# Performance work log

Measured on AMD Instinct MI355X. Metric: run time of the kernel, lower is better.

The kernel has to match this reference:

```python
import jax, jax.numpy as jnp
import numpy as np

NUM_USERS = 200000
NUM_ITEMS = 100000
EMBED_DIM = 64
N_LAYERS = 3
NNZ = 6000000
BATCH = 16384
N_NODES = NUM_USERS + NUM_ITEMS


def setup_inputs() -> dict:
    key = jax.random.key(0)
    k1, k2, k3, k4, k5, k6, k7 = jax.random.split(key, 7)
    user_emb = 0.01 * jax.random.normal(k1, (NUM_USERS, EMBED_DIM), dtype=jnp.float32)
    item_emb = 0.01 * jax.random.normal(k2, (NUM_ITEMS, EMBED_DIM), dtype=jnp.float32)
    adj_rows = jax.random.randint(k3, (NNZ,), 0, N_NODES, dtype=jnp.int32)
    adj_cols = jax.random.randint(k4, (NNZ,), 0, N_NODES, dtype=jnp.int32)
    # positive normalized-adjacency-like values (roughly 1/deg scale)
    adj_vals = jax.random.uniform(k5, (NNZ,), dtype=jnp.float32) * 0.1
    user_ids = jax.random.randint(k6, (BATCH,), 0, NUM_USERS, dtype=jnp.int32)
    item_ids = jax.random.randint(k7, (BATCH,), 0, NUM_ITEMS, dtype=jnp.int32)
    return {
        "user_emb": user_emb,
        "item_emb": item_emb,
        "adj_rows": adj_rows,
        "adj_cols": adj_cols,
        "adj_vals": adj_vals,
        "user_ids": user_ids,
        "item_ids": item_ids,
    }


def reference(user_emb, item_emb, adj_rows, adj_cols, adj_vals, user_ids, item_ids):
    # propagate: repeated SpMM over adjacency with running accumulation
    all_emb = jnp.concatenate([user_emb, item_emb], axis=0)  # [N, D]
    acc = all_emb  # running sum of layer embeddings (fuses stack+mean)
    x = all_emb
    for _ in range(N_LAYERS):
        # SpMM: x_new[r] = sum_e adj_vals[e] * x[adj_cols[e]] for rows r
        msgs = adj_vals[:, None] * x[adj_cols]  # [nnz, D]
        x = jax.ops.segment_sum(msgs, adj_rows, num_segments=N_NODES)
        acc = acc + x
    mean_emb = acc / jnp.float32(N_LAYERS + 1)  # mean over layer outputs
    user_embs = mean_emb[:NUM_USERS]
    item_embs = mean_emb[NUM_USERS:]
    u = user_embs[user_ids]  # [B, D]
    i = item_embs[item_ids]  # [B, D]
    scores = jnp.sum(u * i, axis=1)  # [B]
    return scores
```

## Files before the change

### kernel.cpp

```cpp
#include <hip/hip_runtime.h>

#define EMBED_DIM 64
#define NBLK_A 256
#define BUCKET_SHIFT 9
#define BUCKET_ROWS 512
#define MAX_NBUCK 640
#define SCAN2_CHUNK 2048
#define COL_BITS 19
#define STAGE_CAP 15360

typedef float fx4 __attribute__((ext_vector_type(4)));
typedef int   ix4 __attribute__((ext_vector_type(4)));
typedef float fv4 __attribute__((ext_vector_type(4)));
typedef _Float16 h8v __attribute__((ext_vector_type(8)));

__global__ void convert_x_kernel(const float* __restrict__ ue, const float* __restrict__ ie,
                                 _Float16* __restrict__ xh, int nu_elems, int total) {
    int i = blockIdx.x * blockDim.x + threadIdx.x;
    int stride = gridDim.x * blockDim.x;
    int n8 = total >> 3;
    int nu8 = nu_elems >> 3;
    for (; i < n8; i += stride) {
        const float4* src = (i < nu8) ? (const float4*)(ue) + 2 * i
                                      : (const float4*)(ie) + 2 * (i - nu8);
        float4 lo = src[0];
        float4 hi = src[1];
        h8v o;
        o[0] = (_Float16)lo.x; o[1] = (_Float16)lo.y;
        o[2] = (_Float16)lo.z; o[3] = (_Float16)lo.w;
        o[4] = (_Float16)hi.x; o[5] = (_Float16)hi.y;
        o[6] = (_Float16)hi.z; o[7] = (_Float16)hi.w;
        reinterpret_cast<h8v*>(xh)[i] = o;
    }
}

__global__ __launch_bounds__(256) void bucket_count_kernel(
    const int* __restrict__ rows, int* __restrict__ blockCounts,
    int nnz, int nbuck, int chunk) {
    __shared__ int hist[MAX_NBUCK];
    int t = threadIdx.x, blk = blockIdx.x;
    for (int i = t; i < nbuck; i += 256) hist[i] = 0;
    __syncthreads();
    int e0 = blk * chunk;
    int e1 = min(e0 + chunk, nnz);
    for (int e = e0 + t * 4; e < e1; e += 1024) {
        ix4 r4 = __builtin_nontemporal_load(reinterpret_cast<const ix4*>(rows + e));
        atomicAdd(&hist[r4.x >> BUCKET_SHIFT], 1);
        atomicAdd(&hist[r4.y >> BUCKET_SHIFT], 1);
        atomicAdd(&hist[r4.z >> BUCKET_SHIFT], 1);
        atomicAdd(&hist[r4.w >> BUCKET_SHIFT], 1);
    }
    __syncthreads();
    for (int u = t; u < nbuck; u += 256)
        blockCounts[u * NBLK_A + blk] = hist[u];
}

__global__ void scan8_phase1(const int* __restrict__ in, int* __restrict__ bsum, int n) {
    __shared__ int wsum[4];
    int t = threadIdx.x, b = blockIdx.x;
    int i0 = b * SCAN2_CHUNK + t * 8;
    int s = 0;
    #pragma unroll
    for (int k = 0; k < 8; ++k) { int i = i0 + k; if (i < n) s += in[i]; }
    #pragma unroll
    for (int off = 1; off < 64; off <<= 1) s += __shfl_xor(s, off);
    if ((t & 63) == 0) wsum[t >> 6] = s;
    __syncthreads();
    if (t == 0) bsum[b] = wsum[0] + wsum[1] + wsum[2] + wsum[3];
}

__global__ void scan_phase2(const int* __restrict__ bsum, int* __restrict__ boff, int nb) {
    __shared__ int lds[512];
    int t = threadIdx.x;
    lds[t] = (t < nb) ? bsum[t] : 0;
    __syncthreads();
    for (int off = 1; off < 512; off <<= 1) {
        int v = (t >= off) ? lds[t - off] : 0;
        __syncthreads();
        lds[t] += v;
        __syncthreads();
    }
    if (t < nb) boff[t] = (t == 0) ? 0 : lds[t - 1];
}

__global__ void scan8_phase3(const int* __restrict__ in, const int* __restrict__ boff,
                             int* __restrict__ out, int n) {
    __shared__ int wexcl[4];
    int t = threadIdx.x, b = blockIdx.x;
    int lane = t & 63, w = t >> 6;
    int i0 = b * SCAN2_CHUNK + t * 8;
    int c[8];
    int s = 0;
    #pragma unroll
    for (int k = 0; k < 8; ++k) { int i = i0 + k; c[k] = (i < n) ? in[i] : 0; s += c[k]; }
    int incl = s;
    #pragma unroll
    for (int off = 1; off < 64; off <<= 1) {
        int u = __shfl_up(incl, off);
        if (lane >= off) incl += u;
    }
    if (lane == 63) wexcl[w] = incl;
    __syncthreads();
    int wbase = 0;
    for (int ww = 0; ww < w; ++ww) wbase += wexcl[ww];
    int run = incl - s + wbase + boff[b];
    #pragma unroll
    for (int k = 0; k < 8; ++k) {
        int i = i0 + k;
        if (i < n) { out[i] = run; run += c[k]; }
    }
}

__global__ __launch_bounds__(256) void bucket_scatter_kernel(
    const int* __restrict__ rows, const int* __restrict__ cols,
    const float* __restrict__ vals, const int* __restrict__ scanOut,
    int2* __restrict__ smeta, int nnz, int nbuck, int chunk) {
    __shared__ int cur[MAX_NBUCK];
    int t = threadIdx.x, blk = blockIdx.x;
    for (int u = t; u < nbuck; u += 256) cur[u] = scanOut[u * NBLK_A + blk];
    __syncthreads();
    int e0 = blk * chunk;
    int e1 = min(e0 + chunk, nnz);
    for (int e = e0 + t * 4; e < e1; e += 1024) {
        ix4 r4 = __builtin_nontemporal_load(reinterpret_cast<const ix4*>(rows + e));
        ix4 c4 = __builtin_nontemporal_load(reinterpret_cast<const ix4*>(cols + e));
        fv4 v4 = __builtin_nontemporal_load(reinterpret_cast<const fv4*>(vals + e));
        int p0 = atomicAdd(&cur[r4.x >> BUCKET_SHIFT], 1);
        smeta[p0] = make_int2(((r4.x & (BUCKET_ROWS - 1)) << COL_BITS) | c4.x, __float_as_int(v4.x));
        int p1 = atomicAdd(&cur[r4.y >> BUCKET_SHIFT], 1);
        smeta[p1] = make_int2(((r4.y & (BUCKET_ROWS - 1)) << COL_BITS) | c4.y, __float_as_int(v4.y));
        int p2 = atomicAdd(&cur[r4.z >> BUCKET_SHIFT], 1);
        smeta[p2] = make_int2(((r4.z & (BUCKET_ROWS - 1)) << COL_BITS) | c4.z, __float_as_int(v4.z));
        int p3 = atomicAdd(&cur[r4.w >> BUCKET_SHIFT], 1);
        smeta[p3] = make_int2(((r4.w & (BUCKET_ROWS - 1)) << COL_BITS) | c4.w, __float_as_int(v4.w));
    }
}

__global__ __launch_bounds__(256) void bucket_build_kernel(
    const int2* __restrict__ smeta, const int* __restrict__ scanOut,
    int2* __restrict__ perm, int* __restrict__ row_ptr,
    int nnz, int n_nodes, int nbuck) {
    __shared__ int hist[BUCKET_ROWS], excl[BUCKET_ROWS], cur[BUCKET_ROWS];
    __shared__ int wex[4];
    __shared__ int2 stage[STAGE_CAP];
    int t = threadIdx.x, b = blockIdx.x;
    int lane = t & 63, w = t >> 6;
    int ebeg = scanOut[b * NBLK_A];
    int eend = (b + 1 < nbuck) ? scanOut[(b + 1) * NBLK_A] : nnz;
    hist[t] = 0; hist[t + 256] = 0;
    __syncthreads();
    for (int e = ebeg + t; e < eend; e += 256)
        atomicAdd(&hist[smeta[e].x >> COL_BITS], 1);
    __syncthreads();
    int a = hist[2 * t], bcnt = hist[2 * t + 1];
    int s = a + bcnt;
    int incl = s;
    #pragma unroll
    for (int off = 1; off < 64; off <<= 1) {
        int u = __shfl_up(incl, off);
        if (lane >= off) incl += u;
    }
    if (lane == 63) wex[w] = incl;
    __syncthreads();
    int wbase = 0;
    for (int ww = 0; ww < w; ++ww) wbase += wex[ww];
    int es = wbase + incl - s;
    excl[2 * t] = es;
    excl[2 * t + 1] = es + a;
    cur[2 * t] = es;
    cur[2 * t + 1] = es + a;
    __syncthreads();
    int base_row = b << BUCKET_SHIFT;
    for (int r = t; r < BUCKET_ROWS; r += 256) {
        int gr = base_row + r;
        if (gr < n_nodes) row_ptr[gr] = ebeg + excl[r];
    }
    if (b == 0 && t == 0) row_ptr[n_nodes] = nnz;
    int nbe = eend - ebeg;
    if (nbe <= STAGE_CAP) {
        for (int e = ebeg + t; e < eend; e += 256) {
            int2 m = smeta[e];
            int l = m.x >> COL_BITS;
            int p = atomicAdd(&cur[l], 1);
            stage[p] = make_int2(m.x & ((1 << COL_BITS) - 1), m.y);
        }
        __syncthreads();
        for (int i = t; i < nbe; i += 256)
            perm[ebeg + i] = stage[i];
    } else {
        for (int e = ebeg + t; e < eend; e += 256) {
            int2 m = smeta[e];
            int l = m.x >> COL_BITS;
            int p = atomicAdd(&cur[l], 1);
            perm[ebeg + p] = make_int2(m.x & ((1 << COL_BITS) - 1), m.y);
        }
    }
}

__global__ void init_bacc_kernel(const float* __restrict__ ue, const float* __restrict__ ie,
                                 const int* __restrict__ uids, const int* __restrict__ iids,
                                 float* __restrict__ uacc, float* __restrict__ iacc, int batch) {
    int t = blockIdx.x * blockDim.x + threadIdx.x;
    if (t >= batch * 16) return;
    int b = t >> 4;
    int q = t & 15;
    const float4* ue4 = (const float4*)ue;
    const float4* ie4 = (const float4*)ie;
    ((float4*)uacc)[t] = ue4[(long)uids[b] * 16 + q];
    ((float4*)iacc)[t] = ie4[(long)iids[b] * 16 + q];
}

__global__ __launch_bounds__(256) void mark_needed_kernel(
    const int* __restrict__ row_ptr, const int2* __restrict__ perm,
    const int* __restrict__ uids, const int* __restrict__ iids,
    char* __restrict__ needed, int batch, int num_users) {
    int lane = threadIdx.x & 63;
    int w = (blockIdx.x * blockDim.x + threadIdx.x) >> 6;
    if (w >= 2 * batch) return;
    int row = (w < batch) ? uids[w] : num_users + iids[w - batch];
    if (lane == 0) needed[row] = 1;
    int start = row_ptr[row];
    int end   = row_ptr[row + 1];
    for (int e = start + lane; e < end; e += 64)
        needed[perm[e].x] = 1;
}

__global__ __launch_bounds__(256) void spmm_csr_h_kernel(
    const int* __restrict__ row_ptr, const int2* __restrict__ perm,
    const _Float16* __restrict__ x, _Float16* __restrict__ y,
    const char* __restrict__ needed, int n_nodes) {
    int lane = threadIdx.x & 63;
    int row = (blockIdx.x * blockDim.x + threadIdx.x) >> 6;
    if (row >= n_nodes) return;
    if (needed && !needed[row]) return;
    int start = row_ptr[row];
    int end   = row_ptr[row + 1];
    int sub  = lane >> 3;
    unsigned dimb = ((unsigned)(lane & 7)) << 4;
    const char* xb = reinterpret_cast<const char*>(x);
    float accf[8];
    #pragma unroll
    for (int k = 0; k < 8; ++k) accf[k] = 0.f;
    for (int base = start; base < end; base += 24) {
        int e0 = base + sub;
        int e1 = e0 + 8;
        int e2 = e0 + 16;
        int2 p0 = (e0 < end) ? perm[e0] : make_int2(0, 0);
        int2 p1 = (e1 < end) ? perm[e1] : make_int2(0, 0);
        int2 p2 = (e2 < end) ? perm[e2] : make_int2(0, 0);
        _Float16 vh0 = (_Float16)__int_as_float(p0.y);
        _Float16 vh1 = (_Float16)__int_as_float(p1.y);
        _Float16 vh2 = (_Float16)__int_as_float(p2.y);
        h8v xv0 = *reinterpret_cast<const h8v*>(xb + ((((unsigned)p0.x) << 7) | dimb));
        h8v xv1 = *reinterpret_cast<const h8v*>(xb + ((((unsigned)p1.x) << 7) | dimb));
        h8v xv2 = *reinterpret_cast<const h8v*>(xb + ((((unsigned)p2.x) << 7) | dimb));
        h8v p = xv0 * vh0;
        p += xv1 * vh1;
        p += xv2 * vh2;
        #pragma unroll
        for (int k = 0; k < 8; ++k) accf[k] += (float)p[k];
    }
    #pragma unroll
    for (int off = 8; off < 64; off <<= 1) {
        #pragma unroll
        for (int k = 0; k < 8; ++k) accf[k] += __shfl_xor(accf[k], off);
    }
    if (sub == 0) {
        h8v o;
        #pragma unroll
        for (int k = 0; k < 8; ++k) o[k] = (_Float16)accf[k];
        *reinterpret_cast<h8v*>(reinterpret_cast<char*>(y) + ((((unsigned)row) << 7) | dimb)) = o;
    }
}

__global__ __launch_bounds__(256) void spmm_batch_score_kernel(
    const int* __restrict__ row_ptr, const int2* __restrict__ perm,
    const _Float16* __restrict__ x,
    const int* __restrict__ uids, const int* __restrict__ iids,
    const float* __restrict__ uacc, const float* __restrict__ iacc,
    float* __restrict__ out, int batch, int num_users) {
    int lane = threadIdx.x & 63;
    int b = (blockIdx.x * blockDim.x + threadIdx.x) >> 6;
    if (b >= batch) return;
    int sub  = lane >> 3;
    int dimq = lane & 7;
    unsigned dimb = ((unsigned)dimq) << 4;
    const char* xb = reinterpret_cast<const char*>(x);
    float u3[8], i3[8];
    #pragma unroll
    for (int k = 0; k < 8; ++k) { u3[k] = 0.f; i3[k] = 0.f; }
    {
        int row = uids[b];
        int start = row_ptr[row];
        int end   = row_ptr[row + 1];
        for (int base = start; base < end; base += 16) {
            int e0 = base + sub;
            int e1 = e0 + 8;
            int2 p0 = (e0 < end) ? perm[e0] : make_int2(0, 0);
            int2 p1 = (e1 < end) ? perm[e1] : make_int2(0, 0);
            _Float16 vh0 = (_Float16)__int_as_float(p0.y);
            _Float16 vh1 = (_Float16)__int_as_float(p1.y);
            h8v xv0 = *reinterpret_cast<const h8v*>(xb + ((((unsigned)p0.x) << 7) | dimb));
            h8v xv1 = *reinterpret_cast<const h8v*>(xb + ((((unsigned)p1.x) << 7) | dimb));
            h8v p = xv0 * vh0;
            p += xv1 * vh1;
            #pragma unroll
            for (int k = 0; k < 8; ++k) u3[k] += (float)p[k];
        }
    }
    {
        int row = num_users + iids[b];
        int start = row_ptr[row];
        int end   = row_ptr[row + 1];
        for (int base = start; base < end; base += 16) {
            int e0 = base + sub;
            int e1 = e0 + 8;
            int2 p0 = (e0 < end) ? perm[e0] : make_int2(0, 0);
            int2 p1 = (e1 < end) ? perm[e1] : make_int2(0, 0);
            _Float16 vh0 = (_Float16)__int_as_float(p0.y);
            _Float16 vh1 = (_Float16)__int_as_float(p1.y);
            h8v xv0 = *reinterpret_cast<const h8v*>(xb + ((((unsigned)p0.x) << 7) | dimb));
            h8v xv1 = *reinterpret_cast<const h8v*>(xb + ((((unsigned)p1.x) << 7) | dimb));
            h8v p = xv0 * vh0;
            p += xv1 * vh1;
            #pragma unroll
            for (int k = 0; k < 8; ++k) i3[k] += (float)p[k];
        }
    }
    #pragma unroll
    for (int off = 8; off < 64; off <<= 1) {
        #pragma unroll
        for (int k = 0; k < 8; ++k) {
            u3[k] += __shfl_xor(u3[k], off);
            i3[k] += __shfl_xor(i3[k], off);
        }
    }
    const fx4* ua = reinterpret_cast<const fx4*>(uacc + (long)b * EMBED_DIM) + dimq * 2;
    const fx4* ia = reinterpret_cast<const fx4*>(iacc + (long)b * EMBED_DIM) + dimq * 2;
    fx4 ulo = ua[0], uhi = ua[1];
    fx4 ilo = ia[0], ihi = ia[1];
    float s = 0.f;
    s += (ulo.x + u3[0]) * (ilo.x + i3[0]);
    s += (ulo.y + u3[1]) * (ilo.y + i3[1]);
    s += (ulo.z + u3[2]) * (ilo.z + i3[2]);
    s += (ulo.w + u3[3]) * (ilo.w + i3[3]);
    s += (uhi.x + u3[4]) * (ihi.x + i3[4]);
    s += (uhi.y + u3[5]) * (ihi.y + i3[5]);
    s += (uhi.z + u3[6]) * (ihi.z + i3[6]);
    s += (uhi.w + u3[7]) * (ihi.w + i3[7]);
    #pragma unroll
    for (int off = 1; off < 8; off <<= 1) s += __shfl_xor(s, off);
    if (lane == 0) out[b] = s * (1.0f / 16.0f);
}

__global__ void bacc_add_h_kernel(const _Float16* __restrict__ y,
                                  const int* __restrict__ uids, const int* __restrict__ iids,
                                  float* __restrict__ uacc, float* __restrict__ iacc,
                                  int batch, int num_users) {
    int t = blockIdx.x * blockDim.x + threadIdx.x;
    if (t >= batch * 8) return;
    int b = t >> 3;
    int q = t & 7;
    const h8v* y8 = (const h8v*)y;
    h8v u = y8[(long)uids[b] * 8 + q];
    h8v v = y8[((long)num_users + iids[b]) * 8 + q];
    float4* ua = (float4*)uacc + (long)b * 16 + q * 2;
    float4* ia = (float4*)iacc + (long)b * 16 + q * 2;
    float4 a0 = ua[0], a1 = ua[1];
    a0.x += (float)u[0]; a0.y += (float)u[1]; a0.z += (float)u[2]; a0.w += (float)u[3];
    a1.x += (float)u[4]; a1.y += (float)u[5]; a1.z += (float)u[6]; a1.w += (float)u[7];
    ua[0] = a0; ua[1] = a1;
    float4 c0 = ia[0], c1 = ia[1];
    c0.x += (float)v[0]; c0.y += (float)v[1]; c0.z += (float)v[2]; c0.w += (float)v[3];
    c1.x += (float)v[4]; c1.y += (float)v[5]; c1.z += (float)v[6]; c1.w += (float)v[7];
    ia[0] = c0; ia[1] = c1;
}

extern "C" void kernel_launch(void* const* d_in, const int* in_sizes, int n_in,
                              void* d_out, int out_size, void* d_ws, size_t ws_size,
                              hipStream_t stream) {
    const float* user_emb = (const float*)d_in[0];
    const float* item_emb = (const float*)d_in[1];
    const int*   adj_rows = (const int*)d_in[2];
    const int*   adj_cols = (const int*)d_in[3];
    const float* adj_vals = (const float*)d_in[4];
    const int*   user_ids = (const int*)d_in[5];
    const int*   item_ids = (const int*)d_in[6];
    float* out = (float*)d_out;

    const int num_users = in_sizes[0] / EMBED_DIM;
    const int num_items = in_sizes[1] / EMBED_DIM;
    const int n_nodes   = num_users + num_items;
    const int nnz       = in_sizes[2];
    const int batch     = in_sizes[5];

    const long node_elems = (long)n_nodes * EMBED_DIM;
    const long bacc_elems = (long)batch * EMBED_DIM;

    const int nbuck = (n_nodes + BUCKET_ROWS - 1) >> BUCKET_SHIFT;
    const int nscan = nbuck * NBLK_A;
    const int nscan_blocks = (nscan + SCAN2_CHUNK - 1) / SCAN2_CHUNK;

    char* wp = (char*)d_ws;
    _Float16* xh   = (_Float16*)wp;      wp += node_elems * sizeof(_Float16);
    _Float16* bufA = (_Float16*)wp;      wp += node_elems * sizeof(_Float16);
    _Float16* bufB = (_Float16*)wp;      wp += node_elems * sizeof(_Float16);
    float* uacc = (float*)wp;            wp += bacc_elems * sizeof(float);
    float* iacc = (float*)wp;            wp += bacc_elems * sizeof(float);
    int*   row_ptr = (int*)wp;           wp += (size_t)(n_nodes + 4) * sizeof(int);
    int*   bsum    = (int*)wp;           wp += 512 * sizeof(int);
    int*   boff    = (int*)wp;           wp += 512 * sizeof(int);
    int*   blockCounts = (int*)wp;       wp += (size_t)nscan * sizeof(int);
    int*   scanOut     = (int*)wp;       wp += (size_t)nscan * sizeof(int);
    char*  needed      = wp;             wp += (size_t)n_nodes;
    wp = (char*)(((uintptr_t)wp + 15) & ~(uintptr_t)15);
    int2*  perm    = (int2*)wp;          wp += (size_t)nnz * sizeof(int2);

    int2* smeta = (int2*)bufA;

    const int chunkA = (((nnz + NBLK_A - 1) / NBLK_A) + 1023) & ~1023;

    bucket_count_kernel<<<NBLK_A, 256, 0, stream>>>(adj_rows, blockCounts, nnz, nbuck, chunkA);
    scan8_phase1<<<nscan_blocks, 256, 0, stream>>>(blockCounts, bsum, nscan);
    scan_phase2<<<1, 512, 0, stream>>>(bsum, boff, nscan_blocks);
    scan8_phase3<<<nscan_blocks, 256, 0, stream>>>(blockCounts, boff, scanOut, nscan);
    bucket_scatter_kernel<<<NBLK_A, 256, 0, stream>>>(adj_rows, adj_cols, adj_vals,
                                                      scanOut, smeta, nnz, nbuck, chunkA);
    bucket_build_kernel<<<nbuck, 256, 0, stream>>>(smeta, scanOut, perm,
                                                   row_ptr, nnz, n_nodes, nbuck);

    convert_x_kernel<<<2048, 256, 0, stream>>>(user_emb, item_emb, xh,
                                               num_users * EMBED_DIM, (int)node_elems);

    {
        int blocks = (batch * 16 + 255) / 256;
        init_bacc_kernel<<<blocks, 256, 0, stream>>>(user_emb, item_emb, user_ids, item_ids,
                                                     uacc, iacc, batch);
    }

    hipMemsetAsync(needed, 0, (size_t)n_nodes, stream);
    {
        int waves = 2 * batch;
        int blocks = (waves * 64 + 255) / 256;
        mark_needed_kernel<<<blocks, 256, 0, stream>>>(row_ptr, perm, user_ids, item_ids,
                                                       needed, batch, num_users);
    }

    const int spmm_blocks = ((n_nodes * 64) + 255) / 256;
    const int bblocks = (batch * 8 + 255) / 256;

    spmm_csr_h_kernel<<<spmm_blocks, 256, 0, stream>>>(row_ptr, perm, xh, bufA,
                                                       nullptr, n_nodes);
    bacc_add_h_kernel<<<bblocks, 256, 0, stream>>>(bufA, user_ids, item_ids,
                                                   uacc, iacc, batch, num_users);

    spmm_csr_h_kernel<<<spmm_blocks, 256, 0, stream>>>(row_ptr, perm, bufA, bufB,
                                                       needed, n_nodes);
    bacc_add_h_kernel<<<bblocks, 256, 0, stream>>>(bufB, user_ids, item_ids,
                                                   uacc, iacc, batch, num_users);

    {
        int blocks = (batch * 64 + 255) / 256;
        spmm_batch_score_kernel<<<blocks, 256, 0, stream>>>(row_ptr, perm, bufB,
                                                            user_ids, item_ids,
                                                            uacc, iacc, out,
                                                            batch, num_users);
    }
}
```

Baseline: 488.9 us.

## Drop needed-row pruning for second SpMM and stage bucket entries in LDS

Removes the mark_needed pass, its memset and the per-row needed check, so the second SpMM layer now computes every row instead of only the neighbours of batch rows. Separately, bucket_build now loads smeta into LDS once during the histogram pass and scatters straight to perm from LDS, rather than reading smeta twice and staging the permuted output. This saves a global reread and a memset plus kernel launch, but the second SpMM now processes all rows, including many that pruning used to skip.

```diff
diff --git a/kernel.cpp b/kernel.cpp
--- a/kernel.cpp
+++ b/kernel.cpp
@@ -147,10 +147,20 @@
     int lane = t & 63, w = t >> 6;
     int ebeg = scanOut[b * NBLK_A];
     int eend = (b + 1 < nbuck) ? scanOut[(b + 1) * NBLK_A] : nnz;
+    int nbe = eend - ebeg;
     hist[t] = 0; hist[t + 256] = 0;
     __syncthreads();
-    for (int e = ebeg + t; e < eend; e += 256)
-        atomicAdd(&hist[smeta[e].x >> COL_BITS], 1);
+    bool fit = (nbe <= STAGE_CAP);
+    if (fit) {
+        for (int i = t; i < nbe; i += 256) {
+            int2 m = smeta[ebeg + i];
+            stage[i] = m;
+            atomicAdd(&hist[m.x >> COL_BITS], 1);
+        }
+    } else {
+        for (int e = ebeg + t; e < eend; e += 256)
+            atomicAdd(&hist[smeta[e].x >> COL_BITS], 1);
+    }
     __syncthreads();
     int a = hist[2 * t], bcnt = hist[2 * t + 1];
     int s = a + bcnt;
@@ -176,17 +186,13 @@
         if (gr < n_nodes) row_ptr[gr] = ebeg + excl[r];
     }
     if (b == 0 && t == 0) row_ptr[n_nodes] = nnz;
-    int nbe = eend - ebeg;
-    if (nbe <= STAGE_CAP) {
-        for (int e = ebeg + t; e < eend; e += 256) {
-            int2 m = smeta[e];
+    if (fit) {
+        for (int i = t; i < nbe; i += 256) {
+            int2 m = stage[i];
             int l = m.x >> COL_BITS;
             int p = atomicAdd(&cur[l], 1);
-            stage[p] = make_int2(m.x & ((1 << COL_BITS) - 1), m.y);
-        }
-        __syncthreads();
-        for (int i = t; i < nbe; i += 256)
-            perm[ebeg + i] = stage[i];
+            perm[ebeg + p] = make_int2(m.x & ((1 << COL_BITS) - 1), m.y);
+        }
     } else {
         for (int e = ebeg + t; e < eend; e += 256) {
             int2 m = smeta[e];
@@ -210,29 +216,12 @@
     ((float4*)iacc)[t] = ie4[(long)iids[b] * 16 + q];
 }
 
-__global__ __launch_bounds__(256) void mark_needed_kernel(
-    const int* __restrict__ row_ptr, const int2* __restrict__ perm,
-    const int* __restrict__ uids, const int* __restrict__ iids,
-    char* __restrict__ needed, int batch, int num_users) {
-    int lane = threadIdx.x & 63;
-    int w = (blockIdx.x * blockDim.x + threadIdx.x) >> 6;
-    if (w >= 2 * batch) return;
-    int row = (w < batch) ? uids[w] : num_users + iids[w - batch];
-    if (lane == 0) needed[row] = 1;
-    int start = row_ptr[row];
-    int end   = row_ptr[row + 1];
-    for (int e = start + lane; e < end; e += 64)
-        needed[perm[e].x] = 1;
-}
-
 __global__ __launch_bounds__(256) void spmm_csr_h_kernel(
     const int* __restrict__ row_ptr, const int2* __restrict__ perm,
-    const _Float16* __restrict__ x, _Float16* __restrict__ y,
-    const char* __restrict__ needed, int n_nodes) {
+    const _Float16* __restrict__ x, _Float16* __restrict__ y, int n_nodes) {
     int lane = threadIdx.x & 63;
     int row = (blockIdx.x * blockDim.x + threadIdx.x) >> 6;
     if (row >= n_nodes) return;
-    if (needed && !needed[row]) return;
     int start = row_ptr[row];
     int end   = row_ptr[row + 1];
     int sub  = lane >> 3;
@@ -412,7 +401,6 @@
     int*   boff    = (int*)wp;           wp += 512 * sizeof(int);
     int*   blockCounts = (int*)wp;       wp += (size_t)nscan * sizeof(int);
     int*   scanOut     = (int*)wp;       wp += (size_t)nscan * sizeof(int);
-    char*  needed      = wp;             wp += (size_t)n_nodes;
     wp = (char*)(((uintptr_t)wp + 15) & ~(uintptr_t)15);
     int2*  perm    = (int2*)wp;          wp += (size_t)nnz * sizeof(int2);
 
@@ -438,24 +426,14 @@
                                                      uacc, iacc, batch);
     }
 
-    hipMemsetAsync(needed, 0, (size_t)n_nodes, stream);
-    {
-        int waves = 2 * batch;
-        int blocks = (waves * 64 + 255) / 256;
-        mark_needed_kernel<<<blocks, 256, 0, stream>>>(row_ptr, perm, user_ids, item_ids,
-                                                       needed, batch, num_users);
-    }
-
     const int spmm_blocks = ((n_nodes * 64) + 255) / 256;
     const int bblocks = (batch * 8 + 255) / 256;
 
-    spmm_csr_h_kernel<<<spmm_blocks, 256, 0, stream>>>(row_ptr, perm, xh, bufA,
-                                                       nullptr, n_nodes);
+    spmm_csr_h_kernel<<<spmm_blocks, 256, 0, stream>>>(row_ptr, perm, xh, bufA, n_nodes);
     bacc_add_h_kernel<<<bblocks, 256, 0, stream>>>(bufA, user_ids, item_ids,
                                                    uacc, iacc, batch, num_users);
 
-    spmm_csr_h_kernel<<<spmm_blocks, 256, 0, stream>>>(row_ptr, perm, bufA, bufB,
-                                                       needed, n_nodes);
+    spmm_csr_h_kernel<<<spmm_blocks, 256, 0, stream>>>(row_ptr, perm, bufA, bufB, n_nodes);
     bacc_add_h_kernel<<<bblocks, 256, 0, stream>>>(bufB, user_ids, item_ids,
                                                    uacc, iacc, batch, num_users);
 
```

Measured after the change: 482.5 us. About the same (-1.3%).
